# Kernel optimization log

Measured on AMD Instinct MI355X. Metric: run time of the kernel, lower is better.

The kernel has to match this reference:

```python
import jax, jax.numpy as jnp
import numpy as np

N, E, DIN, H, CHID, COUT, S = 20000, 320000, 128, 4, 64, 64, 32
EPS_BN = 1e-5


def setup_inputs() -> dict:
    key = jax.random.key(0)
    ks = jax.random.split(key, 20)
    g = lambda k, shp, s=0.1: jax.random.normal(k, shp, dtype=jnp.float32) * s
    return {
        "x": jax.random.normal(ks[0], (N, DIN), dtype=jnp.float32),
        "edge_index": jax.random.randint(ks[1], (2, E), 0, N, dtype=jnp.int32),
        "struct_feat": jax.random.normal(ks[2], (N, S), dtype=jnp.float32),
        # GATConv (layer 1)
        "W1": g(ks[3], (H * CHID, DIN)),
        "att_src1": g(ks[4], (1, H, CHID)),
        "att_dst1": g(ks[5], (1, H, CHID)),
        "bias1": jnp.zeros((CHID,), jnp.float32),
        # HybridGateGATLayer (layer 2)
        "W2": g(ks[6], (H * COUT, CHID)),
        "att_src2": g(ks[7], (1, H, COUT)),
        "att_dst2": g(ks[8], (1, H, COUT)),
        "bias2": jnp.zeros((COUT,), jnp.float32),
        "Wt": g(ks[9], (1, S)),
        "bt": jnp.zeros((1,), jnp.float32),
        "We1": g(ks[10], (8, 4), 0.5),
        "be1": jnp.zeros((8,), jnp.float32),
        "We2": g(ks[11], (1, 8), 0.5),
        "be2": jnp.zeros((1,), jnp.float32),
        "betas": jnp.array([1.15, 0.85, 0.1, 0.08, 0.12], jnp.float32),
    }


def _seg_softmax(logits, seg, n):
    m = jax.ops.segment_max(logits, seg, num_segments=n)
    m = jnp.where(jnp.isfinite(m), m, 0.0)
    ex = jnp.exp(logits - m[seg])
    s = jax.ops.segment_sum(ex, seg, num_segments=n)
    return ex / (s[seg] + 1e-16)


def _cos(a, b):
    na = jnp.maximum(jnp.linalg.norm(a, axis=-1), 1e-8)
    nb = jnp.maximum(jnp.linalg.norm(b, axis=-1), 1e-8)
    return (a * b).sum(-1) / (na * nb)


def reference(x, edge_index, struct_feat, W1, att_src1, att_dst1, bias1,
              W2, att_src2, att_dst2, bias2, Wt, bt, We1, be1, We2, be2, betas):
    n = x.shape[0]
    src0, dst0 = edge_index[0], edge_index[1]
    # ---- layer 1: standard GATConv with self loops, concat=False (head mean) ----
    loop = jnp.arange(n, dtype=src0.dtype)
    src = jnp.concatenate([src0, loop])
    dst = jnp.concatenate([dst0, loop])
    h = (x @ W1.T).reshape(n, H, CHID)
    a_s = (h * att_src1).sum(-1)  # [N,H]
    a_d = (h * att_dst1).sum(-1)
    al = jax.nn.leaky_relu(a_s[src] + a_d[dst], 0.2)  # [E+N,H]
    alpha1 = _seg_softmax(al, dst, n)
    out1 = jax.ops.segment_sum(h[src] * alpha1[..., None], dst, num_segments=n)
    h1 = jax.nn.relu(out1.mean(1) + bias1)  # [N,CHID]
    # batch norm (affine=False, batch stats, biased var)
    mu = h1.mean(0)
    var = ((h1 - mu) ** 2).mean(0)
    h1 = (h1 - mu) / jnp.sqrt(var + EPS_BN)
    # ---- layer 2: HybridGateGATLayer (no self loops) ----
    x2 = (h1 @ W2.T).reshape(n, H, COUT)
    node_trust = jax.nn.sigmoid(struct_feat @ Wt.T + bt).squeeze(-1)  # [N]
    as2 = (x2 * att_src2).sum(-1)
    ad2 = (x2 * att_dst2).sum(-1)
    j, i = src0, dst0
    alpha_raw = jax.nn.leaky_relu(as2[j] + ad2[i], 0.2)  # [E,H]
    struct_sim = _cos(struct_feat[j], struct_feat[i])  # [E]
    xf = x2.reshape(n, H * COUT)
    feat_sim = _cos(xf[j], xf[i])
    agreement = struct_sim * feat_sim
    conflict = jnp.abs(struct_sim - feat_sim)
    cues = jnp.stack([struct_sim, feat_sim, agreement, conflict], axis=-1)  # [E,4]
    gate = (jax.nn.relu(cues @ We1.T + be1) @ We2.T + be2).squeeze(-1)
    edge_bonus = jax.nn.sigmoid(gate) * jax.nn.relu(agreement)
    edge_trust = jnp.sqrt(jnp.clip(node_trust[j] * node_trust[i], 0.0))
    trust_bonus = edge_trust * jax.nn.relu(0.5 * (struct_sim + feat_sim))
    gate_logit = (betas[0] * struct_sim + betas[1] * feat_sim + betas[2] * agreement
                  + betas[3] * edge_bonus + betas[4] * trust_bonus)
    alpha2 = _seg_softmax(alpha_raw + gate_logit[:, None], i, n)  # [E,H]
    out2 = jax.ops.segment_sum(x2[j] * alpha2[..., None], i, num_segments=n)
    return out2.mean(1) + bias2  # [N,COUT]
```

## Files before the change

kernel.cpp:

```cpp
#include <hip/hip_runtime.h>
#include <hip/hip_bf16.h>
#include <hip/hip_fp16.h>

#define C_DIN 128
#define C_H 4
#define C_CH 64
#define C_HC 256
#define C_S 32
#define EPB 64
#define ACH 32
#define MBLK 64

typedef __attribute__((ext_vector_type(8))) _Float16 half8;
typedef __attribute__((ext_vector_type(4))) float f32x4;

__device__ __forceinline__ float lrelu(float x) { return x >= 0.f ? x : 0.2f * x; }

__device__ __forceinline__ float sub_sum32(float v) {
#pragma unroll
    for (int off = 16; off > 0; off >>= 1) v += __shfl_xor(v, off);
    return v;
}
__device__ __forceinline__ float sub_max32(float v) {
#pragma unroll
    for (int off = 16; off > 0; off >>= 1) v = fmaxf(v, __shfl_xor(v, off));
    return v;
}

__global__ void k_count(const int* __restrict__ dst, int* __restrict__ deg, int E) {
    int e = blockIdx.x * blockDim.x + threadIdx.x;
    if (e < E) atomicAdd(&deg[dst[e]], 1);
}

__global__ void k_scan(const int* __restrict__ deg, int* __restrict__ row_ptr,
                       int* __restrict__ cursor, int n) {
    __shared__ int part[1024];
    int t = threadIdx.x;
    const int C = (n + 1023) / 1024;
    int base = t * C;
    int s = 0;
    for (int k = 0; k < C; ++k) {
        int idx = base + k;
        if (idx < n) s += deg[idx];
    }
    part[t] = s;
    __syncthreads();
    for (int off = 1; off < 1024; off <<= 1) {
        int v = (t >= off) ? part[t - off] : 0;
        __syncthreads();
        part[t] += v;
        __syncthreads();
    }
    int run = (t == 0) ? 0 : part[t - 1];
    for (int k = 0; k < C; ++k) {
        int idx = base + k;
        if (idx < n) { row_ptr[idx] = run; cursor[idx] = run; run += deg[idx]; }
    }
    if (t == 1023) row_ptr[n] = run;
}

__global__ void k_scatter(const int* __restrict__ src, const int* __restrict__ dst,
                          int* __restrict__ cursor, int* __restrict__ adj_src,
                          int* __restrict__ adj_dst, int E) {
    int e = blockIdx.x * blockDim.x + threadIdx.x;
    if (e < E) {
        int d = dst[e];
        int p = atomicAdd(&cursor[d], 1);
        adj_src[p] = src[e];
        adj_dst[p] = d;
    }
}

__global__ __launch_bounds__(256) void k_gemm1(
    const float* __restrict__ x, const float* __restrict__ W1,
    const float* __restrict__ att_s, const float* __restrict__ att_d,
    __half* __restrict__ hh_out, float* __restrict__ a_s, float* __restrict__ a_d, int n) {
    __shared__ __align__(16) _Float16 bs[4 * 16 * 64 * 8];
    __shared__ __align__(16) _Float16 as_[4 * 4 * 64 * 8];
    int t = threadIdx.x;
    int r0 = blockIdx.x * MBLK;
    {
        int c = t;
        const float4* wrow = (const float4*)(W1 + (size_t)c * C_DIN);
        int nt = c >> 4, cl = c & 15;
#pragma unroll
        for (int ch = 0; ch < 16; ++ch) {
            float4 f0 = wrow[ch * 2], f1 = wrow[ch * 2 + 1];
            int ks = ch >> 2, lg = ch & 3;
            _Float16* dst = &bs[(((ks * 16 + nt) * 64) + (lg * 16 + cl)) * 8];
            dst[0] = (_Float16)f0.x; dst[1] = (_Float16)f0.y;
            dst[2] = (_Float16)f0.z; dst[3] = (_Float16)f0.w;
            dst[4] = (_Float16)f1.x; dst[5] = (_Float16)f1.y;
            dst[6] = (_Float16)f1.z; dst[7] = (_Float16)f1.w;
        }
    }
    {
        int row = t >> 2, q = t & 3;
        int rr = r0 + row;
        int mt = row >> 4, rl = row & 15;
        const float4* xrow = (const float4*)(x + (size_t)rr * C_DIN);
#pragma unroll
        for (int cc = 0; cc < 4; ++cc) {
            int ch = q * 4 + cc;
            float4 f0 = make_float4(0, 0, 0, 0), f1 = make_float4(0, 0, 0, 0);
            if (rr < n) { f0 = xrow[ch * 2]; f1 = xrow[ch * 2 + 1]; }
            int ks = ch >> 2, lg = ch & 3;
            _Float16* dst = &as_[(((ks * 4 + mt) * 64) + (lg * 16 + rl)) * 8];
            dst[0] = (_Float16)f0.x; dst[1] = (_Float16)f0.y;
            dst[2] = (_Float16)f0.z; dst[3] = (_Float16)f0.w;
            dst[4] = (_Float16)f1.x; dst[5] = (_Float16)f1.y;
            dst[6] = (_Float16)f1.z; dst[7] = (_Float16)f1.w;
        }
    }
    __syncthreads();
    int w = t >> 6, l = t & 63;
    f32x4 acc[4][4];
#pragma unroll
    for (int mt = 0; mt < 4; ++mt)
#pragma unroll
        for (int nt = 0; nt < 4; ++nt) acc[mt][nt] = (f32x4){0.f, 0.f, 0.f, 0.f};
#pragma unroll
    for (int ks = 0; ks < 4; ++ks) {
        half8 af[4], bf[4];
#pragma unroll
        for (int mt = 0; mt < 4; ++mt)
            af[mt] = *(const half8*)&as_[(((ks * 4 + mt) * 64) + l) * 8];
#pragma unroll
        for (int nt = 0; nt < 4; ++nt)
            bf[nt] = *(const half8*)&bs[(((ks * 16 + (w * 4 + nt)) * 64) + l) * 8];
#pragma unroll
        for (int mt = 0; mt < 4; ++mt)
#pragma unroll
            for (int nt = 0; nt < 4; ++nt)
                acc[mt][nt] = __builtin_amdgcn_mfma_f32_16x16x32_f16(af[mt], bf[nt],
                                                                     acc[mt][nt], 0, 0, 0);
    }
    int cl = l & 15, rg = l >> 4;
    float atv_s[4], atv_d[4];
#pragma unroll
    for (int nt = 0; nt < 4; ++nt) {
        atv_s[nt] = att_s[w * 64 + nt * 16 + cl];
        atv_d[nt] = att_d[w * 64 + nt * 16 + cl];
    }
#pragma unroll
    for (int mt = 0; mt < 4; ++mt) {
#pragma unroll
        for (int r = 0; r < 4; ++r) {
            int rr = r0 + mt * 16 + rg * 4 + r;
            float vs = 0.f, vd = 0.f;
#pragma unroll
            for (int nt = 0; nt < 4; ++nt) {
                float v = acc[mt][nt][r];
                vs += atv_s[nt] * v;
                vd += atv_d[nt] * v;
                if (rr < n)
                    hh_out[(size_t)rr * C_HC + w * 64 + nt * 16 + cl] = __float2half(v);
            }
#pragma unroll
            for (int off = 1; off < 16; off <<= 1) {
                vs += __shfl_xor(vs, off);
                vd += __shfl_xor(vd, off);
            }
            if (cl == 0 && rr < n) { a_s[rr * C_H + w] = vs; a_d[rr * C_H + w] = vd; }
        }
    }
}

__global__ void k_layer1(const int* __restrict__ row_ptr, const int* __restrict__ adj_src,
                         const __half* __restrict__ hhlf, const float* __restrict__ a_s,
                         const float* __restrict__ a_d, const float* __restrict__ bias1,
                         float* __restrict__ h1) {
    int d = blockIdx.x;
    int t = threadIdx.x, hh = t >> 5, cp = t & 31;
    int beg = row_ptr[d], end = row_ptr[d + 1];
    float adh = a_d[d * C_H + hh];
    float self = lrelu(a_s[d * C_H + hh] + adh);
    float m = self;
    for (int e = beg + cp; e < end; e += 32)
        m = fmaxf(m, lrelu(a_s[adj_src[e] * C_H + hh] + adh));
    m = sub_max32(m);
    float sum = (cp == 0) ? expf(self - m) : 0.f;
    for (int e = beg + cp; e < end; e += 32)
        sum += expf(lrelu(a_s[adj_src[e] * C_H + hh] + adh) - m);
    sum = sub_sum32(sum);
    float inv = 1.f / (sum + 1e-16f);
    __shared__ float alpha_l[C_H][ACH];
    __shared__ int src_l[ACH];
    const __half2* selfrow = (const __half2*)(hhlf + (size_t)d * C_HC + hh * 64);
    float sa = expf(self - m) * inv;
    float2 sv = __half22float2(selfrow[cp]);
    float accx = sa * sv.x, accy = sa * sv.y;
    for (int cbeg = beg; cbeg < end; cbeg += ACH) {
        int cn = min(end - cbeg, ACH);
        __syncthreads();
        if (cp < cn) {
            int s = adj_src[cbeg + cp];
            if (hh == 0) src_l[cp] = s;
            alpha_l[hh][cp] = expf(lrelu(a_s[s * C_H + hh] + adh) - m) * inv;
        }
        __syncthreads();
        for (int i = 0; i < cn; ++i) {
            int s = src_l[i];
            float a = alpha_l[hh][i];
            float2 v = __half22float2(
                *(const __half2*)(hhlf + (size_t)s * C_HC + hh * 64 + cp * 2));
            accx += a * v.x;
            accy += a * v.y;
        }
    }
    __shared__ float2 red[128];
    red[t] = make_float2(accx, accy);
    __syncthreads();
    if (t < 32) {
        float2 r0 = red[t], r1 = red[t + 32], r2 = red[t + 64], r3 = red[t + 96];
        float2 b = *(const float2*)&bias1[t * 2];
        float vx = (r0.x + r1.x + r2.x + r3.x) * 0.25f + b.x;
        float vy = (r0.y + r1.y + r2.y + r3.y) * 0.25f + b.y;
        *(float2*)&h1[(size_t)d * C_CH + t * 2] =
            make_float2(fmaxf(vx, 0.f), fmaxf(vy, 0.f));
    }
}

__global__ void k_bnstats(const float* __restrict__ h1, float* __restrict__ bn, int n) {
    int t = threadIdx.x;
    int c = t & 63, rg = t >> 6;
    float s = 0.f, s2 = 0.f;
    for (int r = blockIdx.x * 4 + rg; r < n; r += gridDim.x * 4) {
        float v = h1[(size_t)r * C_CH + c];
        s += v;
        s2 += v * v;
    }
    __shared__ float ls[256], ls2[256];
    ls[t] = s; ls2[t] = s2;
    __syncthreads();
    if (t < 64) {
        s = ls[t] + ls[t + 64] + ls[t + 128] + ls[t + 192];
        s2 = ls2[t] + ls2[t + 64] + ls2[t + 128] + ls2[t + 192];
        atomicAdd(&bn[c], s);
        atomicAdd(&bn[64 + c], s2);
    }
}

__global__ void k_bnfinal(const float* __restrict__ bn, float* __restrict__ mr, int n) {
    int c = threadIdx.x;
    if (c < 64) {
        float mu = bn[c] / n;
        float var = bn[64 + c] / n - mu * mu;
        mr[c] = mu;
        mr[64 + c] = rsqrtf(var + 1e-5f);
    }
}

__global__ __launch_bounds__(256) void k_gemm2(
    const float* __restrict__ h1, const float* __restrict__ W2,
    const float* __restrict__ att_s, const float* __restrict__ att_d,
    const float* __restrict__ mr, __half* __restrict__ x2h,
    float* __restrict__ as2, float* __restrict__ ad2, float* __restrict__ nf, int n) {
    __shared__ __align__(16) _Float16 bs[2 * 16 * 64 * 8];
    __shared__ __align__(16) _Float16 as_[2 * 4 * 64 * 8];
    __shared__ float nq[64][4];
    int t = threadIdx.x;
    int r0 = blockIdx.x * MBLK;
    {
        int c = t;
        const float4* wrow = (const float4*)(W2 + (size_t)c * C_CH);
        int nt = c >> 4, cl = c & 15;
#pragma unroll
        for (int ch = 0; ch < 8; ++ch) {
            float4 f0 = wrow[ch * 2], f1 = wrow[ch * 2 + 1];
            int ks = ch >> 2, lg = ch & 3;
            _Float16* dst = &bs[(((ks * 16 + nt) * 64) + (lg * 16 + cl)) * 8];
            dst[0] = (_Float16)f0.x; dst[1] = (_Float16)f0.y;
            dst[2] = (_Float16)f0.z; dst[3] = (_Float16)f0.w;
            dst[4] = (_Float16)f1.x; dst[5] = (_Float16)f1.y;
            dst[6] = (_Float16)f1.z; dst[7] = (_Float16)f1.w;
        }
    }
    {
        int row = t >> 2, q = t & 3;
        int rr = r0 + row;
        int mt = row >> 4, rl = row & 15;
        const float4* hrow = (const float4*)(h1 + (size_t)rr * C_CH);
#pragma unroll
        for (int cc = 0; cc < 2; ++cc) {
            int ch = q * 2 + cc;
            float4 f0 = make_float4(0, 0, 0, 0), f1 = make_float4(0, 0, 0, 0);
            if (rr < n) { f0 = hrow[ch * 2]; f1 = hrow[ch * 2 + 1]; }
            const float4 mu0 = *(const float4*)&mr[ch * 8];
            const float4 mu1 = *(const float4*)&mr[ch * 8 + 4];
            const float4 rs0 = *(const float4*)&mr[64 + ch * 8];
            const float4 rs1 = *(const float4*)&mr[64 + ch * 8 + 4];
            int ks = ch >> 2, lg = ch & 3;
            _Float16* dst = &as_[(((ks * 4 + mt) * 64) + (lg * 16 + rl)) * 8];
            dst[0] = (_Float16)((f0.x - mu0.x) * rs0.x);
            dst[1] = (_Float16)((f0.y - mu0.y) * rs0.y);
            dst[2] = (_Float16)((f0.z - mu0.z) * rs0.z);
            dst[3] = (_Float16)((f0.w - mu0.w) * rs0.w);
            dst[4] = (_Float16)((f1.x - mu1.x) * rs1.x);
            dst[5] = (_Float16)((f1.y - mu1.y) * rs1.y);
            dst[6] = (_Float16)((f1.z - mu1.z) * rs1.z);
            dst[7] = (_Float16)((f1.w - mu1.w) * rs1.w);
        }
    }
    __syncthreads();
    int w = t >> 6, l = t & 63;
    f32x4 acc[4][4];
#pragma unroll
    for (int mt = 0; mt < 4; ++mt)
#pragma unroll
        for (int nt = 0; nt < 4; ++nt) acc[mt][nt] = (f32x4){0.f, 0.f, 0.f, 0.f};
#pragma unroll
    for (int ks = 0; ks < 2; ++ks) {
        half8 af[4], bf[4];
#pragma unroll
        for (int mt = 0; mt < 4; ++mt)
            af[mt] = *(const half8*)&as_[(((ks * 4 + mt) * 64) + l) * 8];
#pragma unroll
        for (int nt = 0; nt < 4; ++nt)
            bf[nt] = *(const half8*)&bs[(((ks * 16 + (w * 4 + nt)) * 64) + l) * 8];
#pragma unroll
        for (int mt = 0; mt < 4; ++mt)
#pragma unroll
            for (int nt = 0; nt < 4; ++nt)
                acc[mt][nt] = __builtin_amdgcn_mfma_f32_16x16x32_f16(af[mt], bf[nt],
                                                                     acc[mt][nt], 0, 0, 0);
    }
    int cl = l & 15, rg = l >> 4;
    float atv_s[4], atv_d[4];
#pragma unroll
    for (int nt = 0; nt < 4; ++nt) {
        atv_s[nt] = att_s[w * 64 + nt * 16 + cl];
        atv_d[nt] = att_d[w * 64 + nt * 16 + cl];
    }
#pragma unroll
    for (int mt = 0; mt < 4; ++mt) {
#pragma unroll
        for (int r = 0; r < 4; ++r) {
            int rr = r0 + mt * 16 + rg * 4 + r;
            float vs = 0.f, vd = 0.f, vq = 0.f;
#pragma unroll
            for (int nt = 0; nt < 4; ++nt) {
                float v = acc[mt][nt][r];
                vs += atv_s[nt] * v;
                vd += atv_d[nt] * v;
                vq += v * v;
                if (rr < n)
                    x2h[(size_t)rr * C_HC + w * 64 + nt * 16 + cl] = __float2half(v);
            }
#pragma unroll
            for (int off = 1; off < 16; off <<= 1) {
                vs += __shfl_xor(vs, off);
                vd += __shfl_xor(vd, off);
                vq += __shfl_xor(vq, off);
            }
            if (cl == 0 && rr < n) {
                as2[rr * C_H + w] = vs;
                ad2[rr * C_H + w] = vd;
                nq[mt * 16 + rg * 4 + r][w] = vq;
            }
        }
    }
    __syncthreads();
    if (t < MBLK) {
        int rr = r0 + t;
        if (rr < n) {
            float qq = nq[t][0] + nq[t][1] + nq[t][2] + nq[t][3];
            nf[rr] = fmaxf(sqrtf(qq), 1e-8f);
        }
    }
}

__global__ void k_trust(const float* __restrict__ sf, const float* __restrict__ Wt,
                        const float* __restrict__ bt, float* __restrict__ trust,
                        float* __restrict__ ns, int n) {
    int i = blockIdx.x * blockDim.x + threadIdx.x;
    if (i >= n) return;
    const float4* r4 = (const float4*)(sf + (size_t)i * C_S);
    const float4* w4 = (const float4*)Wt;
    float d = 0.f, q = 0.f;
#pragma unroll
    for (int k = 0; k < 8; ++k) {
        float4 a = r4[k], w = w4[k];
        d += a.x * w.x + a.y * w.y + a.z * w.z + a.w * w.w;
        q += a.x * a.x + a.y * a.y + a.z * a.z + a.w * a.w;
    }
    trust[i] = 1.f / (1.f + expf(-(d + bt[0])));
    ns[i] = fmaxf(sqrtf(q), 1e-8f);
}

__global__ void k_gate(const int* __restrict__ adj_src, const int* __restrict__ adj_dst,
                       const float* __restrict__ sf, const __half* __restrict__ x2h,
                       const float* __restrict__ ns, const float* __restrict__ nf,
                       const float* __restrict__ trust, const float* __restrict__ We1,
                       const float* __restrict__ be1, const float* __restrict__ We2,
                       const float* __restrict__ be2, const float* __restrict__ betas,
                       float* __restrict__ glog, int E) {
    __shared__ float sdL[EPB], fdL[EPB];
    int t = threadIdx.x;
    int w = t >> 6, l = t & 63;
    int g = l >> 4, q = l & 15;
    int e0 = blockIdx.x * EPB;
#pragma unroll
    for (int p = 0; p < 4; ++p) {
        int es = p * 16 + w * 4 + g;
        int e = e0 + es;
        float fd = 0.f, sd = 0.f;
        if (e < E) {
            int j = adj_src[e], i = adj_dst[e];
            const __half2* aj = (const __half2*)(x2h + (size_t)j * C_HC + q * 16);
            const __half2* bi = (const __half2*)(x2h + (size_t)i * C_HC + q * 16);
            float4 ja = *(const float4*)aj;
            float4 jb = *(const float4*)(aj + 4);
            float4 ia = *(const float4*)bi;
            float4 ib = *(const float4*)(bi + 4);
            const __half2* pja = (const __half2*)&ja;
            const __half2* pjb = (const __half2*)&jb;
            const __half2* pia = (const __half2*)&ia;
            const __half2* pib = (const __half2*)&ib;
#pragma unroll
            for (int k = 0; k < 4; ++k) {
                float2 a = __half22float2(pja[k]), b = __half22float2(pia[k]);
                fd += a.x * b.x + a.y * b.y;
                float2 c = __half22float2(pjb[k]), d = __half22float2(pib[k]);
                fd += c.x * d.x + c.y * d.y;
            }
            float2 sj = *(const float2*)(sf + (size_t)j * C_S + q * 2);
            float2 si = *(const float2*)(sf + (size_t)i * C_S + q * 2);
            sd = sj.x * si.x + sj.y * si.y;
        }
#pragma unroll
        for (int off = 1; off < 16; off <<= 1) {
            fd += __shfl_xor(fd, off);
            sd += __shfl_xor(sd, off);
        }
        if (q == 0) { sdL[es] = sd; fdL[es] = fd; }
    }
    __syncthreads();
    if (t < EPB) {
        int e = e0 + t;
        if (e < E) {
            int j = adj_src[e], i = adj_dst[e];
            float ss = sdL[t] / (ns[j] * ns[i]);
            float fs = fdL[t] / (nf[j] * nf[i]);
            float agr = ss * fs;
            float con = fabsf(ss - fs);
            float gate = be2[0];
#pragma unroll
            for (int o = 0; o < 8; ++o) {
                float hdn = We1[o * 4 + 0] * ss + We1[o * 4 + 1] * fs +
                            We1[o * 4 + 2] * agr + We1[o * 4 + 3] * con + be1[o];
                gate += We2[o] * fmaxf(hdn, 0.f);
            }
            float eb = (1.f / (1.f + expf(-gate))) * fmaxf(agr, 0.f);
            float et = sqrtf(fmaxf(trust[j] * trust[i], 0.f));
            float tb = et * fmaxf(0.5f * (ss + fs), 0.f);
            glog[e] = betas[0] * ss + betas[1] * fs + betas[2] * agr +
                      betas[3] * eb + betas[4] * tb;
        }
    }
}

__global__ void k_layer2(const int* __restrict__ row_ptr, const int* __restrict__ adj_src,
                         const __half* __restrict__ x2h, const float* __restrict__ as2,
                         const float* __restrict__ ad2, const float* __restrict__ glog,
                         const float* __restrict__ bias2, float* __restrict__ out) {
    int d = blockIdx.x;
    int t = threadIdx.x, hh = t >> 5, cp = t & 31;
    int beg = row_ptr[d], end = row_ptr[d + 1];
    float adh = ad2[d * C_H + hh];
    float m = -1e30f;
    for (int e = beg + cp; e < end; e += 32)
        m = fmaxf(m, lrelu(as2[adj_src[e] * C_H + hh] + adh) + glog[e]);
    m = sub_max32(m);
    float sum = 0.f;
    for (int e = beg + cp; e < end; e += 32)
        sum += expf(lrelu(as2[adj_src[e] * C_H + hh] + adh) + glog[e] - m);
    sum = sub_sum32(sum);
    float inv = 1.f / (sum + 1e-16f);
    __shared__ float alpha_l[C_H][ACH];
    __shared__ int src_l[ACH];
    float accx = 0.f, accy = 0.f;
    for (int cbeg = beg; cbeg < end; cbeg += ACH) {
        int cn = min(end - cbeg, ACH);
        __syncthreads();
        if (cp < cn) {
            int s = adj_src[cbeg + cp];
            if (hh == 0) src_l[cp] = s;
            alpha_l[hh][cp] =
                expf(lrelu(as2[s * C_H + hh] + adh) + glog[cbeg + cp] - m) * inv;
        }
        __syncthreads();
        for (int i = 0; i < cn; ++i) {
            int s = src_l[i];
            float a = alpha_l[hh][i];
            float2 v = __half22float2(
                *(const __half2*)(x2h + (size_t)s * C_HC + hh * 64 + cp * 2));
            accx += a * v.x;
            accy += a * v.y;
        }
    }
    __shared__ float2 red[128];
    red[t] = make_float2(accx, accy);
    __syncthreads();
    if (t < 32) {
        float2 r0 = red[t], r1 = red[t + 32], r2 = red[t + 64], r3 = red[t + 96];
        float2 b = *(const float2*)&bias2[t * 2];
        float vx = (r0.x + r1.x + r2.x + r3.x) * 0.25f + b.x;
        float vy = (r0.y + r1.y + r2.y + r3.y) * 0.25f + b.y;
        *(float2*)&out[(size_t)d * C_CH + t * 2] = make_float2(vx, vy);
    }
}

static inline size_t al256(size_t x) { return (x + 255) & ~(size_t)255; }

extern "C" void kernel_launch(void* const* d_in, const int* in_sizes, int n_in,
                              void* d_out, int out_size, void* d_ws, size_t ws_size,
                              hipStream_t stream) {
    const float* x      = (const float*)d_in[0];
    const int*   ei     = (const int*)d_in[1];
    const float* sf     = (const float*)d_in[2];
    const float* W1     = (const float*)d_in[3];
    const float* atts1  = (const float*)d_in[4];
    const float* attd1  = (const float*)d_in[5];
    const float* bias1  = (const float*)d_in[6];
    const float* W2     = (const float*)d_in[7];
    const float* atts2  = (const float*)d_in[8];
    const float* attd2  = (const float*)d_in[9];
    const float* bias2  = (const float*)d_in[10];
    const float* Wt     = (const float*)d_in[11];
    const float* bt     = (const float*)d_in[12];
    const float* We1    = (const float*)d_in[13];
    const float* be1    = (const float*)d_in[14];
    const float* We2    = (const float*)d_in[15];
    const float* be2    = (const float*)d_in[16];
    const float* betas  = (const float*)d_in[17];

    const int N = in_sizes[0] / C_DIN;
    const int E = in_sizes[1] / 2;
    const int* srcs = ei;
    const int* dsts = ei + E;

    char* p = (char*)d_ws;
    size_t off = 0;
    auto take = [&](size_t bytes) { char* r = p + off; off = al256(off + bytes); return r; };
    __half* hhlf  = (__half*)take((size_t)N * C_HC * 2);
    float* h1     = (float*)take((size_t)N * C_CH * 4);
    float* a_s1   = (float*)take((size_t)N * C_H * 4);
    float* a_d1   = (float*)take((size_t)N * C_H * 4);
    float* nf     = (float*)take((size_t)N * 4);
    float* ns     = (float*)take((size_t)N * 4);
    float* trust  = (float*)take((size_t)N * 4);
    float* glog   = (float*)take((size_t)E * 4);
    int*   deg    = (int*)take((size_t)N * 4);
    int*   rowp   = (int*)take((size_t)(N + 1) * 4);
    int*   cursor = (int*)take((size_t)N * 4);
    int*   adj_s  = (int*)take((size_t)E * 4);
    int*   adj_d  = (int*)take((size_t)E * 4);
    float* bn     = (float*)take(256 * 4);
    (void)ws_size;
    __half* x2h = hhlf;
    float* as2  = a_s1;
    float* ad2  = a_d1;

    hipMemsetAsync(deg, 0, (size_t)N * 4, stream);
    hipMemsetAsync(bn, 0, 128 * 4, stream);

    k_count<<<(E + 255) / 256, 256, 0, stream>>>(dsts, deg, E);
    k_scan<<<1, 1024, 0, stream>>>(deg, rowp, cursor, N);
    k_scatter<<<(E + 255) / 256, 256, 0, stream>>>(srcs, dsts, cursor, adj_s, adj_d, E);

    k_gemm1<<<(N + MBLK - 1) / MBLK, 256, 0, stream>>>(x, W1, atts1, attd1, hhlf, a_s1, a_d1, N);
    k_layer1<<<N, 128, 0, stream>>>(rowp, adj_s, hhlf, a_s1, a_d1, bias1, h1);
    k_bnstats<<<128, 256, 0, stream>>>(h1, bn, N);
    k_bnfinal<<<1, 64, 0, stream>>>(bn, bn + 128, N);

    k_gemm2<<<(N + MBLK - 1) / MBLK, 256, 0, stream>>>(h1, W2, atts2, attd2, bn + 128, x2h,
                                                       as2, ad2, nf, N);
    k_trust<<<(N + 255) / 256, 256, 0, stream>>>(sf, Wt, bt, trust, ns, N);
    k_gate<<<(E + EPB - 1) / EPB, 256, 0, stream>>>(adj_s, adj_d, sf, x2h, ns, nf, trust,
                                                    We1, be1, We2, be2, betas, glog, E);
    k_layer2<<<N, 128, 0, stream>>>(rowp, adj_s, x2h, as2, ad2, glog, bias2, (float*)d_out);
}
```

Before: 316.6 us.

## Fuse edge gate into layer-2 aggregation and drop max pass in softmax

Merges the per-edge gate kernel and the layer-2 aggregation into one per-destination kernel. Neighbor feature rows are staged in LDS once and reused for both the cosine similarity and the weighted sum, which removes the glog and adj_dst arrays and a second gather. Both attention softmaxes now run in a single pass with no max subtraction, normalizing at the end, which risks exp overflow for large logits. The BN finalize kernel is folded into the gemm2 prologue.

```diff
diff --git a/kernel.cpp b/kernel.cpp
--- a/kernel.cpp
+++ b/kernel.cpp
@@ -7,9 +7,9 @@
 #define C_CH 64
 #define C_HC 256
 #define C_S 32
-#define EPB 64
 #define ACH 32
 #define MBLK 64
+#define XROW 264
 
 typedef __attribute__((ext_vector_type(8))) _Float16 half8;
 typedef __attribute__((ext_vector_type(4))) float f32x4;
@@ -19,11 +19,6 @@
 __device__ __forceinline__ float sub_sum32(float v) {
 #pragma unroll
     for (int off = 16; off > 0; off >>= 1) v += __shfl_xor(v, off);
-    return v;
-}
-__device__ __forceinline__ float sub_max32(float v) {
-#pragma unroll
-    for (int off = 16; off > 0; off >>= 1) v = fmaxf(v, __shfl_xor(v, off));
     return v;
 }
 
@@ -60,14 +55,12 @@
 }
 
 __global__ void k_scatter(const int* __restrict__ src, const int* __restrict__ dst,
-                          int* __restrict__ cursor, int* __restrict__ adj_src,
-                          int* __restrict__ adj_dst, int E) {
+                          int* __restrict__ cursor, int* __restrict__ adj_src, int E) {
     int e = blockIdx.x * blockDim.x + threadIdx.x;
     if (e < E) {
         int d = dst[e];
         int p = atomicAdd(&cursor[d], 1);
         adj_src[p] = src[e];
-        adj_dst[p] = d;
     }
 }
 
@@ -174,29 +167,22 @@
     int t = threadIdx.x, hh = t >> 5, cp = t & 31;
     int beg = row_ptr[d], end = row_ptr[d + 1];
     float adh = a_d[d * C_H + hh];
-    float self = lrelu(a_s[d * C_H + hh] + adh);
-    float m = self;
-    for (int e = beg + cp; e < end; e += 32)
-        m = fmaxf(m, lrelu(a_s[adj_src[e] * C_H + hh] + adh));
-    m = sub_max32(m);
-    float sum = (cp == 0) ? expf(self - m) : 0.f;
-    for (int e = beg + cp; e < end; e += 32)
-        sum += expf(lrelu(a_s[adj_src[e] * C_H + hh] + adh) - m);
-    sum = sub_sum32(sum);
-    float inv = 1.f / (sum + 1e-16f);
+    float p_self = expf(lrelu(a_s[d * C_H + hh] + adh));
     __shared__ float alpha_l[C_H][ACH];
     __shared__ int src_l[ACH];
     const __half2* selfrow = (const __half2*)(hhlf + (size_t)d * C_HC + hh * 64);
-    float sa = expf(self - m) * inv;
     float2 sv = __half22float2(selfrow[cp]);
-    float accx = sa * sv.x, accy = sa * sv.y;
+    float accx = p_self * sv.x, accy = p_self * sv.y;
+    float s_part = (cp == 0) ? p_self : 0.f;
     for (int cbeg = beg; cbeg < end; cbeg += ACH) {
         int cn = min(end - cbeg, ACH);
         __syncthreads();
         if (cp < cn) {
             int s = adj_src[cbeg + cp];
             if (hh == 0) src_l[cp] = s;
-            alpha_l[hh][cp] = expf(lrelu(a_s[s * C_H + hh] + adh) - m) * inv;
+            float p = expf(lrelu(a_s[s * C_H + hh] + adh));
+            alpha_l[hh][cp] = p;
+            s_part += p;
         }
         __syncthreads();
         for (int i = 0; i < cn; ++i) {
@@ -208,8 +194,10 @@
             accy += a * v.y;
         }
     }
+    float s = sub_sum32(s_part);
+    float inv = 1.f / (s + 1e-16f);
     __shared__ float2 red[128];
-    red[t] = make_float2(accx, accy);
+    red[t] = make_float2(accx * inv, accy * inv);
     __syncthreads();
     if (t < 32) {
         float2 r0 = red[t], r1 = red[t + 32], r2 = red[t + 64], r3 = red[t + 96];
@@ -241,20 +229,10 @@
     }
 }
 
-__global__ void k_bnfinal(const float* __restrict__ bn, float* __restrict__ mr, int n) {
-    int c = threadIdx.x;
-    if (c < 64) {
-        float mu = bn[c] / n;
-        float var = bn[64 + c] / n - mu * mu;
-        mr[c] = mu;
-        mr[64 + c] = rsqrtf(var + 1e-5f);
-    }
-}
-
 __global__ __launch_bounds__(256) void k_gemm2(
     const float* __restrict__ h1, const float* __restrict__ W2,
     const float* __restrict__ att_s, const float* __restrict__ att_d,
-    const float* __restrict__ mr, __half* __restrict__ x2h,
+    const float* __restrict__ bn, __half* __restrict__ x2h,
     float* __restrict__ as2, float* __restrict__ ad2, float* __restrict__ nf, int n) {
     __shared__ __align__(16) _Float16 bs[2 * 16 * 64 * 8];
     __shared__ __align__(16) _Float16 as_[2 * 4 * 64 * 8];
@@ -280,16 +258,27 @@
         int row = t >> 2, q = t & 3;
         int rr = r0 + row;
         int mt = row >> 4, rl = row & 15;
+        const float invN = 1.f / (float)n;
         const float4* hrow = (const float4*)(h1 + (size_t)rr * C_CH);
 #pragma unroll
         for (int cc = 0; cc < 2; ++cc) {
             int ch = q * 2 + cc;
             float4 f0 = make_float4(0, 0, 0, 0), f1 = make_float4(0, 0, 0, 0);
             if (rr < n) { f0 = hrow[ch * 2]; f1 = hrow[ch * 2 + 1]; }
-            const float4 mu0 = *(const float4*)&mr[ch * 8];
-            const float4 mu1 = *(const float4*)&mr[ch * 8 + 4];
-            const float4 rs0 = *(const float4*)&mr[64 + ch * 8];
-            const float4 rs1 = *(const float4*)&mr[64 + ch * 8 + 4];
+            float4 s0 = *(const float4*)&bn[ch * 8];
+            float4 s1 = *(const float4*)&bn[ch * 8 + 4];
+            float4 q0 = *(const float4*)&bn[64 + ch * 8];
+            float4 q1 = *(const float4*)&bn[64 + ch * 8 + 4];
+            float4 mu0 = make_float4(s0.x * invN, s0.y * invN, s0.z * invN, s0.w * invN);
+            float4 mu1 = make_float4(s1.x * invN, s1.y * invN, s1.z * invN, s1.w * invN);
+            float4 rs0 = make_float4(rsqrtf(q0.x * invN - mu0.x * mu0.x + 1e-5f),
+                                     rsqrtf(q0.y * invN - mu0.y * mu0.y + 1e-5f),
+                                     rsqrtf(q0.z * invN - mu0.z * mu0.z + 1e-5f),
+                                     rsqrtf(q0.w * invN - mu0.w * mu0.w + 1e-5f));
+            float4 rs1 = make_float4(rsqrtf(q1.x * invN - mu1.x * mu1.x + 1e-5f),
+                                     rsqrtf(q1.y * invN - mu1.y * mu1.y + 1e-5f),
+                                     rsqrtf(q1.z * invN - mu1.z * mu1.z + 1e-5f),
+                                     rsqrtf(q1.w * invN - mu1.w * mu1.w + 1e-5f));
             int ks = ch >> 2, lg = ch & 3;
             _Float16* dst = &as_[(((ks * 4 + mt) * 64) + (lg * 16 + rl)) * 8];
             dst[0] = (_Float16)((f0.x - mu0.x) * rs0.x);
@@ -388,60 +377,67 @@
     ns[i] = fmaxf(sqrtf(q), 1e-8f);
 }
 
-__global__ void k_gate(const int* __restrict__ adj_src, const int* __restrict__ adj_dst,
-                       const float* __restrict__ sf, const __half* __restrict__ x2h,
-                       const float* __restrict__ ns, const float* __restrict__ nf,
-                       const float* __restrict__ trust, const float* __restrict__ We1,
-                       const float* __restrict__ be1, const float* __restrict__ We2,
-                       const float* __restrict__ be2, const float* __restrict__ betas,
-                       float* __restrict__ glog, int E) {
-    __shared__ float sdL[EPB], fdL[EPB];
-    int t = threadIdx.x;
-    int w = t >> 6, l = t & 63;
-    int g = l >> 4, q = l & 15;
-    int e0 = blockIdx.x * EPB;
-#pragma unroll
-    for (int p = 0; p < 4; ++p) {
-        int es = p * 16 + w * 4 + g;
-        int e = e0 + es;
+__global__ __launch_bounds__(128) void k_fused2(
+    const int* __restrict__ row_ptr, const int* __restrict__ adj_src,
+    const float* __restrict__ sf, const __half* __restrict__ x2h,
+    const float* __restrict__ ns, const float* __restrict__ nf,
+    const float* __restrict__ trust, const float* __restrict__ as2,
+    const float* __restrict__ ad2, const float* __restrict__ We1,
+    const float* __restrict__ be1, const float* __restrict__ We2,
+    const float* __restrict__ be2, const float* __restrict__ betas,
+    const float* __restrict__ bias2, float* __restrict__ out) {
+    __shared__ __align__(16) _Float16 xrows[ACH * XROW];
+    __shared__ __align__(16) _Float16 xd[C_HC];
+    __shared__ float sfd[C_S];
+    __shared__ float pbuf[C_H][ACH];
+    __shared__ float2 red[128];
+    int d = blockIdx.x;
+    int t = threadIdx.x, hh = t >> 5, cp = t & 31;
+    int beg = row_ptr[d], end = row_ptr[d + 1];
+    if (t < 32) {
+        ((float4*)xd)[t] = ((const float4*)(x2h + (size_t)d * C_HC))[t];
+    } else if (t < 40) {
+        ((float4*)sfd)[t - 32] = ((const float4*)(sf + (size_t)d * C_S))[t - 32];
+    }
+    float4 ad2d = *(const float4*)&ad2[d * C_H];
+    float nsd = ns[d], nfd = nf[d], trd = trust[d];
+    int er = t >> 2, q = t & 3;
+    float accx = 0.f, accy = 0.f, s_part = 0.f;
+    for (int cbeg = beg; cbeg < end; cbeg += ACH) {
+        int cn = min(end - cbeg, ACH);
+        __syncthreads();
+        int sload = 0;
+        if (q == 0 && er < cn) sload = adj_src[cbeg + er];
+        int j = __shfl(sload, (t & 63) & ~3);
+        if (er < cn) {
+            const float4* grow = (const float4*)(x2h + (size_t)j * C_HC) + q * 8;
+            float4* lrow = (float4*)&xrows[er * XROW + q * 64];
+#pragma unroll
+            for (int u = 0; u < 8; ++u) lrow[u] = grow[u];
+        }
+        __syncthreads();
         float fd = 0.f, sd = 0.f;
-        if (e < E) {
-            int j = adj_src[e], i = adj_dst[e];
-            const __half2* aj = (const __half2*)(x2h + (size_t)j * C_HC + q * 16);
-            const __half2* bi = (const __half2*)(x2h + (size_t)i * C_HC + q * 16);
-            float4 ja = *(const float4*)aj;
-            float4 jb = *(const float4*)(aj + 4);
-            float4 ia = *(const float4*)bi;
-            float4 ib = *(const float4*)(bi + 4);
-            const __half2* pja = (const __half2*)&ja;
-            const __half2* pjb = (const __half2*)&jb;
-            const __half2* pia = (const __half2*)&ia;
-            const __half2* pib = (const __half2*)&ib;
-#pragma unroll
-            for (int k = 0; k < 4; ++k) {
-                float2 a = __half22float2(pja[k]), b = __half22float2(pia[k]);
+        if (er < cn) {
+            const _Float16* xr = &xrows[er * XROW];
+#pragma unroll
+            for (int m = 0; m < 32; ++m) {
+                float2 a = __half22float2(*(const __half2*)&xr[m * 8 + q * 2]);
+                float2 b = __half22float2(*(const __half2*)&xd[m * 8 + q * 2]);
                 fd += a.x * b.x + a.y * b.y;
-                float2 c = __half22float2(pjb[k]), d = __half22float2(pib[k]);
-                fd += c.x * d.x + c.y * d.y;
-            }
-            float2 sj = *(const float2*)(sf + (size_t)j * C_S + q * 2);
-            float2 si = *(const float2*)(sf + (size_t)i * C_S + q * 2);
-            sd = sj.x * si.x + sj.y * si.y;
-        }
-#pragma unroll
-        for (int off = 1; off < 16; off <<= 1) {
-            fd += __shfl_xor(fd, off);
-            sd += __shfl_xor(sd, off);
-        }
-        if (q == 0) { sdL[es] = sd; fdL[es] = fd; }
-    }
-    __syncthreads();
-    if (t < EPB) {
-        int e = e0 + t;
-        if (e < E) {
-            int j = adj_src[e], i = adj_dst[e];
-            float ss = sdL[t] / (ns[j] * ns[i]);
-            float fs = fdL[t] / (nf[j] * nf[i]);
+            }
+            const float4* sj = (const float4*)(sf + (size_t)j * C_S) + q * 2;
+#pragma unroll
+            for (int u = 0; u < 2; ++u) {
+                float4 a = sj[u];
+                float4 b = *(const float4*)&sfd[q * 8 + u * 4];
+                sd += a.x * b.x + a.y * b.y + a.z * b.z + a.w * b.w;
+            }
+        }
+        fd += __shfl_xor(fd, 1); fd += __shfl_xor(fd, 2);
+        sd += __shfl_xor(sd, 1); sd += __shfl_xor(sd, 2);
+        if (q == 0 && er < cn) {
+            float ss = sd / (nsd * ns[j]);
+            float fs = fd / (nfd * nf[j]);
             float agr = ss * fs;
             float con = fabsf(ss - fs);
             float gate = be2[0];
@@ -452,55 +448,29 @@
                 gate += We2[o] * fmaxf(hdn, 0.f);
             }
             float eb = (1.f / (1.f + expf(-gate))) * fmaxf(agr, 0.f);
-            float et = sqrtf(fmaxf(trust[j] * trust[i], 0.f));
+            float et = sqrtf(fmaxf(trd * trust[j], 0.f));
             float tb = et * fmaxf(0.5f * (ss + fs), 0.f);
-            glog[e] = betas[0] * ss + betas[1] * fs + betas[2] * agr +
+            float g = betas[0] * ss + betas[1] * fs + betas[2] * agr +
                       betas[3] * eb + betas[4] * tb;
-        }
-    }
-}
-
-__global__ void k_layer2(const int* __restrict__ row_ptr, const int* __restrict__ adj_src,
-                         const __half* __restrict__ x2h, const float* __restrict__ as2,
-                         const float* __restrict__ ad2, const float* __restrict__ glog,
-                         const float* __restrict__ bias2, float* __restrict__ out) {
-    int d = blockIdx.x;
-    int t = threadIdx.x, hh = t >> 5, cp = t & 31;
-    int beg = row_ptr[d], end = row_ptr[d + 1];
-    float adh = ad2[d * C_H + hh];
-    float m = -1e30f;
-    for (int e = beg + cp; e < end; e += 32)
-        m = fmaxf(m, lrelu(as2[adj_src[e] * C_H + hh] + adh) + glog[e]);
-    m = sub_max32(m);
-    float sum = 0.f;
-    for (int e = beg + cp; e < end; e += 32)
-        sum += expf(lrelu(as2[adj_src[e] * C_H + hh] + adh) + glog[e] - m);
-    sum = sub_sum32(sum);
-    float inv = 1.f / (sum + 1e-16f);
-    __shared__ float alpha_l[C_H][ACH];
-    __shared__ int src_l[ACH];
-    float accx = 0.f, accy = 0.f;
-    for (int cbeg = beg; cbeg < end; cbeg += ACH) {
-        int cn = min(end - cbeg, ACH);
-        __syncthreads();
-        if (cp < cn) {
-            int s = adj_src[cbeg + cp];
-            if (hh == 0) src_l[cp] = s;
-            alpha_l[hh][cp] =
-                expf(lrelu(as2[s * C_H + hh] + adh) + glog[cbeg + cp] - m) * inv;
+            float4 asj = *(const float4*)&as2[j * C_H];
+            pbuf[0][er] = expf(lrelu(asj.x + ad2d.x) + g);
+            pbuf[1][er] = expf(lrelu(asj.y + ad2d.y) + g);
+            pbuf[2][er] = expf(lrelu(asj.z + ad2d.z) + g);
+            pbuf[3][er] = expf(lrelu(asj.w + ad2d.w) + g);
         }
         __syncthreads();
         for (int i = 0; i < cn; ++i) {
-            int s = src_l[i];
-            float a = alpha_l[hh][i];
+            float pv = pbuf[hh][i];
             float2 v = __half22float2(
-                *(const __half2*)(x2h + (size_t)s * C_HC + hh * 64 + cp * 2));
-            accx += a * v.x;
-            accy += a * v.y;
-        }
-    }
-    __shared__ float2 red[128];
-    red[t] = make_float2(accx, accy);
+                *(const __half2*)&xrows[i * XROW + hh * 64 + cp * 2]);
+            accx += pv * v.x;
+            accy += pv * v.y;
+        }
+        if (cp < cn) s_part += pbuf[hh][cp];
+    }
+    float s = sub_sum32(s_part);
+    float inv = 1.f / (s + 1e-16f);
+    red[t] = make_float2(accx * inv, accy * inv);
     __syncthreads();
     if (t < 32) {
         float2 r0 = red[t], r1 = red[t + 32], r2 = red[t + 64], r3 = red[t + 96];
@@ -550,13 +520,11 @@
     float* nf     = (float*)take((size_t)N * 4);
     float* ns     = (float*)take((size_t)N * 4);
     float* trust  = (float*)take((size_t)N * 4);
-    float* glog   = (float*)take((size_t)E * 4);
     int*   deg    = (int*)take((size_t)N * 4);
     int*   rowp   = (int*)take((size_t)(N + 1) * 4);
     int*   cursor = (int*)take((size_t)N * 4);
     int*   adj_s  = (int*)take((size_t)E * 4);
-    int*   adj_d  = (int*)take((size_t)E * 4);
-    float* bn     = (float*)take(256 * 4);
+    float* bn     = (float*)take(128 * 4);
     (void)ws_size;
     __half* x2h = hhlf;
     float* as2  = a_s1;
@@ -567,17 +535,15 @@
 
     k_count<<<(E + 255) / 256, 256, 0, stream>>>(dsts, deg, E);
     k_scan<<<1, 1024, 0, stream>>>(deg, rowp, cursor, N);
-    k_scatter<<<(E + 255) / 256, 256, 0, stream>>>(srcs, dsts, cursor, adj_s, adj_d, E);
+    k_scatter<<<(E + 255) / 256, 256, 0, stream>>>(srcs, dsts, cursor, adj_s, E);
 
     k_gemm1<<<(N + MBLK - 1) / MBLK, 256, 0, stream>>>(x, W1, atts1, attd1, hhlf, a_s1, a_d1, N);
     k_layer1<<<N, 128, 0, stream>>>(rowp, adj_s, hhlf, a_s1, a_d1, bias1, h1);
     k_bnstats<<<128, 256, 0, stream>>>(h1, bn, N);
-    k_bnfinal<<<1, 64, 0, stream>>>(bn, bn + 128, N);
-
-    k_gemm2<<<(N + MBLK - 1) / MBLK, 256, 0, stream>>>(h1, W2, atts2, attd2, bn + 128, x2h,
+
+    k_gemm2<<<(N + MBLK - 1) / MBLK, 256, 0, stream>>>(h1, W2, atts2, attd2, bn, x2h,
                                                        as2, ad2, nf, N);
     k_trust<<<(N + 255) / 256, 256, 0, stream>>>(sf, Wt, bt, trust, ns, N);
-    k_gate<<<(E + EPB - 1) / EPB, 256, 0, stream>>>(adj_s, adj_d, sf, x2h, ns, nf, trust,
-                                                    We1, be1, We2, be2, betas, glog, E);
-    k_layer2<<<N, 128, 0, stream>>>(rowp, adj_s, x2h, as2, ad2, glog, bias2, (float*)d_out);
-}
+    k_fused2<<<N, 128, 0, stream>>>(rowp, adj_s, sf, x2h, ns, nf, trust, as2, ad2,
+                                    We1, be1, We2, be2, betas, bias2, (float*)d_out);
+}
```

Result: no change. 311.5 us (-1.6%).
